# Kernel optimization log

Measured on AMD Instinct MI355X. Metric: run time of the kernel, lower is better.

## Reference

```python
import jax, jax.numpy as jnp
import numpy as np

N_HOPS = 2
TOPK = 10
LAMBDA = 0.5  # lambda_coeff
N_ENT = 8192
N_USR = 16384
CHANNEL = 64
N_EDGE = 1000000
NNZ = 500000
N_REL = 9


def _l2norm(x, eps=1e-12):
    # F.normalize: x / max(||x||, eps) per row
    n = jnp.linalg.norm(x, axis=-1, keepdims=True)
    return x / jnp.maximum(n, eps)


def build_adj(context, topk):
    n = context.shape[0]
    cn = context / jnp.linalg.norm(context, axis=-1, keepdims=True)
    sim = cn @ cn.T                                   # [N,N]
    knn_val, knn_ind = jax.lax.top_k(sim, topk)        # [N,topk]
    rows = jnp.repeat(jnp.arange(n), topk)
    cols = knn_ind.reshape(-1)
    vals = knn_val.reshape(-1)
    rowsum = knn_val.sum(axis=1)                       # sparse row sums
    dinv = rowsum ** -0.5
    vals = dinv[rows] * vals * dinv[cols]              # D^-1/2 A D^-1/2
    return jnp.zeros((n, n), context.dtype).at[rows, cols].add(vals)


def aggregate(entity_emb, user_emb, head, tail, i_rows, i_cols, inter_vals, weight, edge_type):
    n_ent = entity_emb.shape[0]
    n_usr = user_emb.shape[0]
    rel = weight[edge_type - 1]                        # [E,C]
    h_emb = entity_emb[head]
    t_emb = entity_emb[tail]
    neigh = t_emb * rel                                # [E,C]
    # attention weight: (||h*r|| * ||t*r||)^2 per edge
    att = (jnp.linalg.norm(h_emb * rel, axis=1) * jnp.linalg.norm(t_emb * rel, axis=1)) ** 2
    # scatter_softmax over head segments
    m = jax.ops.segment_max(att, head, num_segments=n_ent)
    e = jnp.exp(att - m[head])
    denom = jax.ops.segment_sum(e, head, num_segments=n_ent)
    w = (e / denom[head])[:, None]                     # [E,1], broadcast == expand
    entity_agg = jax.ops.segment_sum(w * neigh, head, num_segments=n_ent)
    # sparse mm: interact_mat @ entity_emb
    user_agg = jax.ops.segment_sum(inter_vals[:, None] * entity_emb[i_cols], i_rows, num_segments=n_usr)
    score = jax.nn.softmax(user_emb @ weight.T, axis=-1)
    user_agg = user_agg + (score @ weight) * user_agg
    return entity_agg, user_agg


def setup_inputs() -> dict:
    key = jax.random.key(0)
    k = jax.random.split(key, 7)
    user_emb = jax.random.normal(k[0], (N_USR, CHANNEL), jnp.float32) * 0.1
    entity_emb = jax.random.normal(k[1], (N_ENT, CHANNEL), jnp.float32) * 0.1
    edge_index = jax.random.randint(k[2], (2, N_EDGE), 0, N_ENT)
    edge_type = jax.random.randint(k[3], (N_EDGE,), 0, N_REL - 1) + 1  # in [1, n_relations-1]
    inter_rows = jax.random.randint(k[4], (NNZ,), 0, N_USR)
    inter_cols = jax.random.randint(k[5], (NNZ,), 0, N_ENT)
    inter_indices = jnp.stack([inter_rows, inter_cols], axis=0)
    inter_vals = jax.random.uniform(k[6], (NNZ,), jnp.float32)
    # xavier-uniform-like relation weight
    bound = float(np.sqrt(6.0 / (N_REL - 1 + CHANNEL)))
    weight = jax.random.uniform(jax.random.fold_in(key, 7), (N_REL - 1, CHANNEL), jnp.float32, -bound, bound)
    return {"user_emb": user_emb, "entity_emb": entity_emb, "edge_index": edge_index,
            "edge_type": edge_type, "inter_indices": inter_indices,
            "inter_vals": inter_vals, "weight": weight}


def reference(user_emb, entity_emb, edge_index, edge_type, inter_indices, inter_vals, weight):
    head, tail = edge_index[0], edge_index[1]
    i_rows, i_cols = inter_indices[0], inter_indices[1]
    origin_item_adj = build_adj(entity_emb, TOPK)
    entity_res_emb = entity_emb
    user_res_emb = user_emb
    for _ in range(N_HOPS):
        entity_emb, user_emb = aggregate(entity_emb, user_emb, head, tail,
                                         i_rows, i_cols, inter_vals, weight, edge_type)
        entity_emb = _l2norm(entity_emb)
        user_emb = _l2norm(user_emb)
        entity_res_emb = entity_res_emb + entity_emb
        user_res_emb = user_res_emb + user_emb
    item_adj = (1.0 - LAMBDA) * build_adj(entity_res_emb, TOPK) + LAMBDA * origin_item_adj
    return entity_res_emb, user_res_emb, item_adj
```

## Files before the change

### kernel.cpp

```cpp
#include <hip/hip_runtime.h>
#include <hip/hip_bf16.h>

#define N_ENT   8192
#define N_USR   16384
#define CH      64
#define N_EDGEC 1000000
#define NNZC    500000
#define TOPKC   10
#define NRELM1  8
#define KSPLIT  384
#define BKS     96

typedef __bf16 bf16x8 __attribute__((ext_vector_type(8)));
typedef float  f32x4  __attribute__((ext_vector_type(4)));

static __device__ __forceinline__ float waveReduceSum(float v){
#pragma unroll
  for(int o=1;o<64;o<<=1) v += __shfl_xor(v,o,64);
  return v;
}
static __device__ __forceinline__ float waveReduceMax(float v){
#pragma unroll
  for(int o=1;o<64;o<<=1) v = fmaxf(v, __shfl_xor(v,o,64));
  return v;
}
static __device__ __forceinline__ int waveReduceMaxI(int v){
#pragma unroll
  for(int o=1;o<64;o<<=1){ int t=__shfl_xor(v,o,64); v = t>v? t: v; }
  return v;
}
static __device__ __forceinline__ unsigned long long u64max(unsigned long long a, unsigned long long b){
  return a>b? a: b;
}
static __device__ __forceinline__ unsigned mapf(float v){
  unsigned u = __float_as_uint(v);
  return (u & 0x80000000u) ? ~u : (u | 0x80000000u);
}
static __device__ __forceinline__ int vbin(float v){
  int b = (int)fmaf(v, 1023.5f, 1023.5f);
  return min(max(b, 0), 2047);
}
static __device__ __forceinline__ ushort f2bf(float x){
  unsigned u = __float_as_uint(x);
  return (ushort)((u + 0x7FFFu + ((u>>16)&1u)) >> 16);
}
static __device__ __forceinline__ float bf2f(ushort h){
  return __uint_as_float((unsigned)h<<16);
}

__global__ void k_hist(const int* __restrict__ keys, int n, int* __restrict__ hist){
  int i = blockIdx.x*blockDim.x + threadIdx.x;
  int stride = gridDim.x*blockDim.x;
  for(; i<n; i+=stride) atomicAdd(&hist[keys[i]], 1);
}

__global__ __launch_bounds__(1024) void k_scan(const int* __restrict__ hist,
                                               int* __restrict__ start,
                                               int* __restrict__ cursor, int n){
  __shared__ int part[1024];
  int t = threadIdx.x;
  int chunk = n/1024;
  int base = t*chunk;
  int s = 0;
  for(int i=0;i<chunk;i++) s += hist[base+i];
  part[t] = s; __syncthreads();
  for(int off=1; off<1024; off<<=1){
    int v = (t>=off) ? part[t-off] : 0;
    __syncthreads();
    part[t] += v;
    __syncthreads();
  }
  int run = (t==0) ? 0 : part[t-1];
  for(int i=0;i<chunk;i++){
    start[base+i] = run; cursor[base+i] = run;
    run += hist[base+i];
  }
  if(t==1023) start[n] = run;
}

__global__ void k_scatter_sortE(const int* __restrict__ head,
                                const int* __restrict__ tail,
                                const int* __restrict__ etype, int n,
                                int* __restrict__ cursor, int* __restrict__ trS){
  int i = blockIdx.x*blockDim.x + threadIdx.x;
  int stride = gridDim.x*blockDim.x;
  for(; i<n; i+=stride){
    int pos = atomicAdd(&cursor[head[i]], 1);
    trS[pos] = (tail[i] & 8191) | ((etype[i]-1)<<13);
  }
}

__global__ void k_scatter_sortU(const int* __restrict__ irows,
                                const int* __restrict__ icols,
                                const float* __restrict__ ivals, int n,
                                int* __restrict__ cursor,
                                int* __restrict__ icolsS, float* __restrict__ ivalsS){
  int i = blockIdx.x*blockDim.x + threadIdx.x;
  int stride = gridDim.x*blockDim.x;
  for(; i<n; i+=stride){
    int pos = atomicAdd(&cursor[irows[i]], 1);
    icolsS[pos] = icols[i];
    ivalsS[pos] = ivals[i];
  }
}

__global__ __launch_bounds__(256) void k_split(const float* __restrict__ in,
                                               ushort* __restrict__ outA,
                                               ushort* __restrict__ outB){
  int wave = threadIdx.x>>6, lane = threadIdx.x&63;
  int r = blockIdx.x*4 + wave;
  float v = in[(size_t)r*CH+lane];
  float ss = waveReduceSum(v*v);
  float x = v / sqrtf(ss);
  ushort h = f2bf(x);
  float r1 = x - bf2f(h);
  ushort m = f2bf(r1);
  float r2 = r1 - bf2f(m);
  ushort l = f2bf(r2);
  ushort* oA = outA + (size_t)r*KSPLIT;
  ushort* oB = outB + (size_t)r*KSPLIT;
  oA[lane]     =h; oA[64+lane] =h; oA[128+lane]=m;
  oA[192+lane] =l; oA[256+lane]=h; oA[320+lane]=m;
  oB[lane]     =h; oB[64+lane] =m; oB[128+lane]=h;
  oB[192+lane] =h; oB[256+lane]=l; oB[320+lane]=m;
}

__global__ __launch_bounds__(256) void k_gemm_bf16(const ushort* __restrict__ A,
                                                   const ushort* __restrict__ B,
                                                   float* __restrict__ C){
  __shared__ ushort As[128*BKS];
  __shared__ ushort Bs[128*BKS];
  const int tid = threadIdx.x, lane = tid&63, wid = tid>>6;
  const int bi = blockIdx.y*128, bj = blockIdx.x*128;
  const int wr = (wid>>1)*64, wc = (wid&1)*64;
  const int r16 = lane&15, kg = lane>>4;

  f32x4 acc[4][4] = {};

  const uint4* gA = (const uint4*)A + (size_t)bi*(KSPLIT/8);
  const uint4* gB = (const uint4*)B + (size_t)bj*(KSPLIT/8);
  const int row2 = tid>>1, half = tid&1;

  for(int s=0; s<KSPLIT/BKS; ++s){
    __syncthreads();
#pragma unroll
    for(int jj=0;jj<6;jj++){
      *(uint4*)&As[row2*BKS + half*48 + jj*8] = gA[row2*(KSPLIT/8) + s*12 + half*6 + jj];
      *(uint4*)&Bs[row2*BKS + half*48 + jj*8] = gB[row2*(KSPLIT/8) + s*12 + half*6 + jj];
    }
    __syncthreads();
#pragma unroll
    for(int kk=0;kk<3;kk++){
      bf16x8 a[4], b[4];
#pragma unroll
      for(int m=0;m<4;m++)
        a[m] = *(const bf16x8*)&As[(wr+m*16+r16)*BKS + kk*32 + kg*8];
#pragma unroll
      for(int n=0;n<4;n++)
        b[n] = *(const bf16x8*)&Bs[(wc+n*16+r16)*BKS + kk*32 + kg*8];
#pragma unroll
      for(int m=0;m<4;m++)
#pragma unroll
        for(int n=0;n<4;n++)
          acc[m][n] = __builtin_amdgcn_mfma_f32_16x16x32_bf16(a[m], b[n], acc[m][n], 0,0,0);
    }
  }

#pragma unroll
  for(int m=0;m<4;m++){
#pragma unroll
    for(int n=0;n<4;n++){
      size_t base = (size_t)(bi + wr + m*16 + kg*4)*N_ENT + (bj + wc + n*16 + r16);
      C[base]          = acc[m][n][0];
      C[base+N_ENT]    = acc[m][n][1];
      C[base+2*N_ENT]  = acc[m][n][2];
      C[base+3*N_ENT]  = acc[m][n][3];
    }
  }
}

#define CANDCAP 256
__global__ __launch_bounds__(64) void k_topk(const float* __restrict__ S,
                                             int* __restrict__ knn_idx,
                                             float* __restrict__ knn_val,
                                             float* __restrict__ rowsum){
  const int row = blockIdx.x;
  const int lane = threadIdx.x;
  const float4* s4 = (const float4*)(S + (size_t)row*N_ENT);

  __shared__ int hist[2048];
  __shared__ unsigned long long cand[CANDCAP];
  __shared__ int cnt;
#pragma unroll
  for(int i=lane;i<2048;i+=64) hist[i]=0;
  if(lane==0) cnt=0;
  __syncthreads();

  for(int it=0; it<N_ENT/256; ++it){
    float4 v = s4[it*64+lane];
    atomicAdd(&hist[vbin(v.x)],1);
    atomicAdd(&hist[vbin(v.y)],1);
    atomicAdd(&hist[vbin(v.z)],1);
    atomicAdd(&hist[vbin(v.w)],1);
  }
  __syncthreads();

  int base = lane*32;
  int s = 0;
#pragma unroll
  for(int j=0;j<32;j++) s += hist[base+j];
  int ss = s;
#pragma unroll
  for(int off=1; off<64; off<<=1){
    int t = __shfl_down(ss, off, 64);
    if(lane+off<64) ss += t;
  }
  int above = ss - s;
  int B_local = 0;
  if(ss >= TOPKC && above < TOPKC){
    int running = above;
    for(int j=31;j>=0;--j){
      running += hist[base+j];
      if(running >= TOPKC){ B_local = base+j; break; }
    }
  }
  int B = waveReduceMaxI(B_local);

  for(int it=0; it<N_ENT/256; ++it){
    int vi = it*64+lane;
    float4 v = s4[vi];
    int c0 = vi*4;
    float vv[4] = {v.x,v.y,v.z,v.w};
#pragma unroll
    for(int j=0;j<4;j++){
      if(vbin(vv[j]) >= B){
        int pos = atomicAdd(&cnt,1);
        if(pos < CANDCAP)
          cand[pos] = ((unsigned long long)mapf(vv[j])<<32)
                    | (unsigned long long)(0xFFFFFFFFu - (unsigned)(c0+j));
      }
    }
  }
  __syncthreads();
  int n = cnt;

  if(n <= CANDCAP){
    unsigned long long c0 = (lane      < n) ? cand[lane]       : 0ull;
    unsigned long long c1 = (lane+64   < n) ? cand[lane+64]    : 0ull;
    unsigned long long c2 = (lane+128  < n) ? cand[lane+128]   : 0ull;
    unsigned long long c3 = (lane+192  < n) ? cand[lane+192]   : 0ull;
    float rs = 0.f;
    for(int sel=0; sel<TOPKC; ++sel){
      unsigned long long m = u64max(u64max(c0,c1), u64max(c2,c3));
#pragma unroll
      for(int o=1;o<64;o<<=1) m = u64max(m, __shfl_xor(m,o,64));
      if(c0==m) c0=0ull; else if(c1==m) c1=0ull;
      else if(c2==m) c2=0ull; else if(c3==m) c3=0ull;
      if(lane==0){
        unsigned mk = (unsigned)(m>>32);
        unsigned uo = (mk & 0x80000000u) ? (mk ^ 0x80000000u) : ~mk;
        float v = __uint_as_float(uo);
        int col = (int)(0xFFFFFFFFu - (unsigned)(m & 0xFFFFFFFFu));
        knn_idx[row*TOPKC+sel] = col;
        knn_val[row*TOPKC+sel] = v;
        rs += v;
      }
    }
    if(lane==0) rowsum[row] = rs;
  } else {
    unsigned long long loc[TOPKC];
#pragma unroll
    for(int i=0;i<TOPKC;i++) loc[i]=0ull;
    for(int it=0; it<N_ENT/256; ++it){
      int vi = it*64+lane;
      float4 v = s4[vi];
      int c0i = vi*4;
      float vv[4] = {v.x,v.y,v.z,v.w};
#pragma unroll
      for(int j=0;j<4;j++){
        unsigned u = mapf(vv[j]);
        unsigned long long key = ((unsigned long long)u<<32)
                               | (unsigned long long)(0xFFFFFFFFu - (unsigned)(c0i+j));
        if(key > loc[TOPKC-1]){
          unsigned long long t = key;
#pragma unroll
          for(int z=0; z<TOPKC; ++z){
            if(t > loc[z]){ unsigned long long tmp=loc[z]; loc[z]=t; t=tmp; }
          }
        }
      }
    }
    float rs = 0.f;
    for(int sel=0; sel<TOPKC; ++sel){
      unsigned long long m = loc[0];
#pragma unroll
      for(int o=1;o<64;o<<=1) m = u64max(m, __shfl_xor(m,o,64));
      if(loc[0] == m){
#pragma unroll
        for(int z=0;z<TOPKC-1;++z) loc[z]=loc[z+1];
        loc[TOPKC-1]=0ull;
      }
      if(lane==0){
        unsigned mk = (unsigned)(m>>32);
        unsigned uo = (mk & 0x80000000u) ? (mk ^ 0x80000000u) : ~mk;
        float v = __uint_as_float(uo);
        int col = (int)(0xFFFFFFFFu - (unsigned)(m & 0xFFFFFFFFu));
        knn_idx[row*TOPKC+sel] = col;
        knn_val[row*TOPKC+sel] = v;
        rs += v;
      }
    }
    if(lane==0) rowsum[row] = rs;
  }
}

__global__ __launch_bounds__(256) void k_q(const float* __restrict__ ent,
                                           const float* __restrict__ W,
                                           float* __restrict__ q){
  int wave=threadIdx.x>>6, lane=threadIdx.x&63;
  int r = blockIdx.x*4+wave;
  if(r>=N_ENT) return;
  float x = ent[(size_t)r*CH+lane];
#pragma unroll
  for(int rel=0; rel<NRELM1; rel++){
    float tt = x*W[rel*CH+lane];
    float s = waveReduceSum(tt*tt);
    if(lane==0) q[r*NRELM1+rel]=s;
  }
}

__global__ __launch_bounds__(256) void k_edge_agg(
    const int* __restrict__ trS, const int* __restrict__ startE,
    const float* __restrict__ ent, const float* __restrict__ W,
    const float* __restrict__ q, float* __restrict__ wbuf,
    float* __restrict__ agg){
  int wave=threadIdx.x>>6, lane=threadIdx.x&63;
  int h = blockIdx.x*4+wave;
  if(h>=N_ENT) return;
  int s = startE[h], e2 = startE[h+1];

  float qh[NRELM1];
#pragma unroll
  for(int r=0;r<NRELM1;r++) qh[r] = q[h*NRELM1+r];

  float mx = 0.f;
  for(int p=s+lane; p<e2; p+=64){
    int tr = trS[p];
    int tl = tr & 8191, r = tr>>13;
    float att = qh[r]*q[tl*NRELM1+r];
    wbuf[p] = att;
    mx = fmaxf(mx, att);
  }
  mx = waveReduceMax(mx);

  float dn = 0.f;
  for(int p=s+lane; p<e2; p+=64){
    float e = expf(wbuf[p]-mx);
    wbuf[p] = e;
    dn += e;
  }
  dn = waveReduceSum(dn);
  float inv = (dn>0.f) ? 1.f/dn : 0.f;

  float wr[NRELM1];
#pragma unroll
  for(int r=0;r<NRELM1;r++) wr[r] = W[r*CH+lane];
  float acc = 0.f;
  for(int p=s; p<e2; p++){
    int tr = trS[p];
    int tl = tr & 8191, r = tr>>13;
    float wgt = wbuf[p]*inv;
    acc = fmaf(wgt*wr[r], ent[(size_t)tl*CH+lane], acc);
  }
  agg[(size_t)h*CH+lane] = acc;
}

__global__ __launch_bounds__(256) void k_user(
    const int* __restrict__ icolsS, const float* __restrict__ ivalsS,
    const int* __restrict__ startU,
    const float* __restrict__ ent, const float* __restrict__ W,
    float* __restrict__ usr, float* __restrict__ usr_res){
  int wave=threadIdx.x>>6, lane=threadIdx.x&63;
  int u = blockIdx.x*4+wave;
  if(u>=N_USR) return;
  float ue = usr[(size_t)u*CH+lane];
  float l[NRELM1];
#pragma unroll
  for(int r=0;r<NRELM1;r++) l[r] = waveReduceSum(ue*W[r*CH+lane]);
  float lm = l[0];
#pragma unroll
  for(int r=1;r<NRELM1;r++) lm = fmaxf(lm,l[r]);
  float se=0.f;
#pragma unroll
  for(int r=0;r<NRELM1;r++){ l[r]=expf(l[r]-lm); se+=l[r]; }
  float inv = 1.f/se;
  float g = 0.f;
#pragma unroll
  for(int r=0;r<NRELM1;r++) g = fmaf(l[r]*inv, W[r*CH+lane], g);
  float acc=0.f;
  int s=startU[u], e2=startU[u+1];
  for(int p=s;p<e2;p++){
    acc = fmaf(ivalsS[p], ent[(size_t)icolsS[p]*CH+lane], acc);
  }
  float res = acc*(1.f+g);
  float nrm = sqrtf(waveReduceSum(res*res));
  float outv = res / fmaxf(nrm, 1e-12f);
  usr_res[(size_t)u*CH+lane] += outv;
  usr[(size_t)u*CH+lane] = outv;
}

__global__ __launch_bounds__(256) void k_entfin(const float* __restrict__ agg,
                                                float* __restrict__ cur,
                                                float* __restrict__ res){
  int wave=threadIdx.x>>6, lane=threadIdx.x&63;
  int r = blockIdx.x*4+wave;
  if(r>=N_ENT) return;
  float v = agg[(size_t)r*CH+lane];
  float nrm = sqrtf(waveReduceSum(v*v));
  float outv = v / fmaxf(nrm, 1e-12f);
  cur[(size_t)r*CH+lane]=outv;
  res[(size_t)r*CH+lane]+=outv;
}

__global__ __launch_bounds__(256) void k_write_adj(
    const int* __restrict__ ki0, const float* __restrict__ kv0,
    const float* __restrict__ rs0,
    const int* __restrict__ ki1, const float* __restrict__ kv1,
    const float* __restrict__ rs1,
    float* __restrict__ adj){
  const int row = blockIdx.x;
  const int t = threadIdx.x;
  __shared__ int   cols[2*TOPKC];
  __shared__ float vals[2*TOPKC];

  if(t < TOPKC){
    int c = ki1[row*TOPKC+t];
    cols[t] = c;
    vals[t] = 0.5f * kv1[row*TOPKC+t] / (sqrtf(rs1[row]) * sqrtf(rs1[c]));
  } else if(t < 2*TOPKC){
    int i = t - TOPKC;
    int c = ki0[row*TOPKC+i];
    cols[t] = c;
    vals[t] = 0.5f * kv0[row*TOPKC+i] / (sqrtf(rs0[row]) * sqrtf(rs0[c]));
  }
  __syncthreads();
  if(t==0){
    for(int i=TOPKC;i<2*TOPKC;i++){
      int c = cols[i];
      for(int j=0;j<TOPKC;j++){
        if(cols[j]==c){ vals[j]+=vals[i]; cols[i]=-1; break; }
      }
    }
  }
  __syncthreads();

  float4* adj4 = (float4*)(adj + (size_t)row*N_ENT);
  float4 z = {0.f,0.f,0.f,0.f};
#pragma unroll
  for(int k=0;k<8;k++) adj4[k*256 + t] = z;
  __syncthreads();
  if(t < 2*TOPKC){
    int c = cols[t];
    if(c >= 0) adj[(size_t)row*N_ENT + c] = vals[t];
  }
}

extern "C" void kernel_launch(void* const* d_in, const int* in_sizes, int n_in,
                              void* d_out, int out_size, void* d_ws, size_t ws_size,
                              hipStream_t stream){
  const float* user_emb   = (const float*)d_in[0];
  const float* entity_emb = (const float*)d_in[1];
  const int*   edge_index = (const int*)d_in[2];
  const int*   edge_type  = (const int*)d_in[3];
  const int*   inter_idx  = (const int*)d_in[4];
  const float* inter_vals = (const float*)d_in[5];
  const float* W          = (const float*)d_in[6];

  const int* head  = edge_index;
  const int* tail  = edge_index + N_EDGEC;
  const int* irows = inter_idx;
  const int* icols = inter_idx + NNZC;

  float* out     = (float*)d_out;
  float* ent_res = out;
  float* usr_res = out + (size_t)N_ENT*CH;
  float* adj     = out + (size_t)N_ENT*CH + (size_t)N_USR*CH;

  char* wp = (char*)d_ws;
  auto alloc = [&](size_t bytes)->void*{
    void* p = (void*)wp; wp += (bytes+255)/256*256; return p;
  };
  ushort* abufA  = (ushort*)alloc((size_t)N_ENT*KSPLIT*2);
  ushort* abufB  = (ushort*)alloc((size_t)N_ENT*KSPLIT*2);
  float* cur_ent = (float*)alloc((size_t)N_ENT*CH*4);
  float* cur_usr = (float*)alloc((size_t)N_USR*CH*4);
  float* agg     = (float*)alloc((size_t)N_ENT*CH*4);
  float* q       = (float*)alloc((size_t)N_ENT*NRELM1*4);
  int*   histE   = (int*)alloc((size_t)N_ENT*4);
  int*   startE  = (int*)alloc((size_t)(N_ENT+1)*4);
  int*   cursorE = (int*)alloc((size_t)N_ENT*4);
  int*   trS     = (int*)alloc((size_t)N_EDGEC*4);
  int*   histU   = (int*)alloc((size_t)N_USR*4);
  int*   startU  = (int*)alloc((size_t)(N_USR+1)*4);
  int*   cursorU = (int*)alloc((size_t)N_USR*4);
  int*   icolsS  = (int*)alloc((size_t)NNZC*4);
  float* ivalsS  = (float*)alloc((size_t)NNZC*4);
  int*   knn_idx0= (int*)alloc((size_t)N_ENT*TOPKC*4);
  float* knn_val0= (float*)alloc((size_t)N_ENT*TOPKC*4);
  float* rowsum0 = (float*)alloc((size_t)N_ENT*4);
  int*   knn_idx1= (int*)alloc((size_t)N_ENT*TOPKC*4);
  float* knn_val1= (float*)alloc((size_t)N_ENT*TOPKC*4);
  float* rowsum1 = (float*)alloc((size_t)N_ENT*4);

  float* wbuf = adj;

  hipMemsetAsync(histE, 0, (size_t)N_ENT*4, stream);
  hipMemsetAsync(histU, 0, (size_t)N_USR*4, stream);
  hipMemcpyAsync(ent_res, entity_emb, (size_t)N_ENT*CH*4, hipMemcpyDeviceToDevice, stream);
  hipMemcpyAsync(usr_res, user_emb,   (size_t)N_USR*CH*4, hipMemcpyDeviceToDevice, stream);
  hipMemcpyAsync(cur_ent, entity_emb, (size_t)N_ENT*CH*4, hipMemcpyDeviceToDevice, stream);
  hipMemcpyAsync(cur_usr, user_emb,   (size_t)N_USR*CH*4, hipMemcpyDeviceToDevice, stream);

  k_hist<<<1024,256,0,stream>>>(head, N_EDGEC, histE);
  k_hist<<<512,256,0,stream>>>(irows, NNZC, histU);
  k_scan<<<1,1024,0,stream>>>(histE, startE, cursorE, N_ENT);
  k_scan<<<1,1024,0,stream>>>(histU, startU, cursorU, N_USR);
  k_scatter_sortE<<<1024,256,0,stream>>>(head, tail, edge_type, N_EDGEC, cursorE, trS);
  k_scatter_sortU<<<512,256,0,stream>>>(irows, icols, inter_vals, NNZC, cursorU, icolsS, ivalsS);

  dim3 gg(N_ENT/128, N_ENT/128);

  k_split<<<N_ENT/4,256,0,stream>>>(entity_emb, abufA, abufB);
  k_gemm_bf16<<<gg,256,0,stream>>>(abufA, abufB, adj);
  k_topk<<<N_ENT,64,0,stream>>>(adj, knn_idx0, knn_val0, rowsum0);

  for(int hop=0; hop<2; ++hop){
    k_q<<<N_ENT/4,256,0,stream>>>(cur_ent, W, q);
    k_edge_agg<<<N_ENT/4,256,0,stream>>>(trS, startE, cur_ent, W, q, wbuf, agg);
    k_user<<<N_USR/4,256,0,stream>>>(icolsS, ivalsS, startU, cur_ent, W, cur_usr, usr_res);
    k_entfin<<<N_ENT/4,256,0,stream>>>(agg, cur_ent, ent_res);
  }

  k_split<<<N_ENT/4,256,0,stream>>>(ent_res, abufA, abufB);
  k_gemm_bf16<<<gg,256,0,stream>>>(abufA, abufB, adj);
  k_topk<<<N_ENT,64,0,stream>>>(adj, knn_idx1, knn_val1, rowsum1);

  k_write_adj<<<N_ENT,256,0,stream>>>(knn_idx0, knn_val0, rowsum0,
                                      knn_idx1, knn_val1, rowsum1, adj);
}
```

Measured before the change: 0.9998 ms.

## Prune top-k scan using per-tile row maxima computed in GEMM epilogue

The GEMM epilogue now reduces each 128-column tile's row maximum and writes it to a rowmax buffer. The top-k kernel takes the 10th-largest tile maximum as a lower bound on the threshold and rereads only the tiles whose maximum reaches it, instead of two full histogram passes over each 8192-wide row. This cuts top-k memory traffic sharply. It adds shuffles, two syncs and a small store to the GEMM, and it depends on the threshold keeping candidates under the cap or taking the fallback path.

New measurement: 847.1 us. 1.18x faster.

```diff
diff --git a/kernel.cpp b/kernel.cpp
--- a/kernel.cpp
+++ b/kernel.cpp
@@ -10,6 +10,7 @@
 #define NRELM1  8
 #define KSPLIT  384
 #define BKS     96
+#define NTILE   64
 
 typedef __bf16 bf16x8 __attribute__((ext_vector_type(8)));
 typedef float  f32x4  __attribute__((ext_vector_type(4)));
@@ -22,11 +23,6 @@
 static __device__ __forceinline__ float waveReduceMax(float v){
 #pragma unroll
   for(int o=1;o<64;o<<=1) v = fmaxf(v, __shfl_xor(v,o,64));
-  return v;
-}
-static __device__ __forceinline__ int waveReduceMaxI(int v){
-#pragma unroll
-  for(int o=1;o<64;o<<=1){ int t=__shfl_xor(v,o,64); v = t>v? t: v; }
   return v;
 }
 static __device__ __forceinline__ unsigned long long u64max(unsigned long long a, unsigned long long b){
@@ -36,9 +32,9 @@
   unsigned u = __float_as_uint(v);
   return (u & 0x80000000u) ? ~u : (u | 0x80000000u);
 }
-static __device__ __forceinline__ int vbin(float v){
-  int b = (int)fmaf(v, 1023.5f, 1023.5f);
-  return min(max(b, 0), 2047);
+static __device__ __forceinline__ float unmapf(unsigned mk){
+  unsigned uo = (mk & 0x80000000u) ? (mk ^ 0x80000000u) : ~mk;
+  return __uint_as_float(uo);
 }
 static __device__ __forceinline__ ushort f2bf(float x){
   unsigned u = __float_as_uint(x);
@@ -127,7 +123,8 @@
 
 __global__ __launch_bounds__(256) void k_gemm_bf16(const ushort* __restrict__ A,
                                                    const ushort* __restrict__ B,
-                                                   float* __restrict__ C){
+                                                   float* __restrict__ C,
+                                                   float* __restrict__ rowmax){
   __shared__ ushort As[128*BKS];
   __shared__ ushort Bs[128*BKS];
   const int tid = threadIdx.x, lane = tid&63, wid = tid>>6;
@@ -177,10 +174,45 @@
       C[base+3*N_ENT]  = acc[m][n][3];
     }
   }
+
+  float tmax[4][4];
+#pragma unroll
+  for(int m=0;m<4;m++){
+#pragma unroll
+    for(int rg=0;rg<4;rg++){
+      float v = acc[m][0][rg];
+      v = fmaxf(v, acc[m][1][rg]);
+      v = fmaxf(v, acc[m][2][rg]);
+      v = fmaxf(v, acc[m][3][rg]);
+#pragma unroll
+      for(int o=1;o<16;o<<=1) v = fmaxf(v, __shfl_xor(v, o, 64));
+      tmax[m][rg] = v;
+    }
+  }
+  __syncthreads();
+  float* rm = (float*)As;
+  if(((wid&1)==0) && r16==0){
+#pragma unroll
+    for(int m=0;m<4;m++)
+#pragma unroll
+      for(int rg=0;rg<4;rg++)
+        rm[wr + m*16 + kg*4 + rg] = tmax[m][rg];
+  }
+  __syncthreads();
+  if(((wid&1)==1) && r16==0){
+#pragma unroll
+    for(int m=0;m<4;m++)
+#pragma unroll
+      for(int rg=0;rg<4;rg++){
+        int rrow = wr + m*16 + kg*4 + rg;
+        rowmax[(size_t)(bi+rrow)*NTILE + blockIdx.x] = fmaxf(tmax[m][rg], rm[rrow]);
+      }
+  }
 }
 
 #define CANDCAP 256
 __global__ __launch_bounds__(64) void k_topk(const float* __restrict__ S,
+                                             const float* __restrict__ rowmax,
                                              int* __restrict__ knn_idx,
                                              float* __restrict__ knn_val,
                                              float* __restrict__ rowsum){
@@ -188,52 +220,36 @@
   const int lane = threadIdx.x;
   const float4* s4 = (const float4*)(S + (size_t)row*N_ENT);
 
-  __shared__ int hist[2048];
   __shared__ unsigned long long cand[CANDCAP];
-  __shared__ int cnt;
-#pragma unroll
-  for(int i=lane;i<2048;i+=64) hist[i]=0;
-  if(lane==0) cnt=0;
-  __syncthreads();
-
-  for(int it=0; it<N_ENT/256; ++it){
-    float4 v = s4[it*64+lane];
-    atomicAdd(&hist[vbin(v.x)],1);
-    atomicAdd(&hist[vbin(v.y)],1);
-    atomicAdd(&hist[vbin(v.z)],1);
-    atomicAdd(&hist[vbin(v.w)],1);
-  }
-  __syncthreads();
-
-  int base = lane*32;
-  int s = 0;
-#pragma unroll
-  for(int j=0;j<32;j++) s += hist[base+j];
-  int ss = s;
-#pragma unroll
-  for(int off=1; off<64; off<<=1){
-    int t = __shfl_down(ss, off, 64);
-    if(lane+off<64) ss += t;
-  }
-  int above = ss - s;
-  int B_local = 0;
-  if(ss >= TOPKC && above < TOPKC){
-    int running = above;
-    for(int j=31;j>=0;--j){
-      running += hist[base+j];
-      if(running >= TOPKC){ B_local = base+j; break; }
-    }
-  }
-  int B = waveReduceMaxI(B_local);
-
-  for(int it=0; it<N_ENT/256; ++it){
-    int vi = it*64+lane;
-    float4 v = s4[vi];
-    int c0 = vi*4;
+  __shared__ int tlist[NTILE];
+  __shared__ int cnt, tcnt;
+  if(lane==0){ cnt=0; tcnt=0; }
+  __syncthreads();
+
+  float tm = rowmax[(size_t)row*NTILE + lane];
+  unsigned long long work = ((unsigned long long)mapf(tm)<<32) | (unsigned)lane;
+  unsigned long long w = 0;
+  for(int sel=0; sel<TOPKC; ++sel){
+    w = work;
+#pragma unroll
+    for(int o=1;o<64;o<<=1) w = u64max(w, __shfl_xor(w,o,64));
+    if(work == w) work = 0ull;
+  }
+  float tauf = unmapf((unsigned)(w>>32));
+
+  if(tm >= tauf){ int p = atomicAdd(&tcnt,1); tlist[p] = lane; }
+  __syncthreads();
+  int nt = tcnt;
+
+  for(int i = (lane>>5); i < nt; i += 2){
+    int t  = tlist[i];
+    int fo = lane&31;
+    float4 v = s4[t*32 + fo];
+    int c0 = t*128 + fo*4;
     float vv[4] = {v.x,v.y,v.z,v.w};
 #pragma unroll
     for(int j=0;j<4;j++){
-      if(vbin(vv[j]) >= B){
+      if(vv[j] >= tauf){
         int pos = atomicAdd(&cnt,1);
         if(pos < CANDCAP)
           cand[pos] = ((unsigned long long)mapf(vv[j])<<32)
@@ -257,9 +273,7 @@
       if(c0==m) c0=0ull; else if(c1==m) c1=0ull;
       else if(c2==m) c2=0ull; else if(c3==m) c3=0ull;
       if(lane==0){
-        unsigned mk = (unsigned)(m>>32);
-        unsigned uo = (mk & 0x80000000u) ? (mk ^ 0x80000000u) : ~mk;
-        float v = __uint_as_float(uo);
+        float v = unmapf((unsigned)(m>>32));
         int col = (int)(0xFFFFFFFFu - (unsigned)(m & 0xFFFFFFFFu));
         knn_idx[row*TOPKC+sel] = col;
         knn_val[row*TOPKC+sel] = v;
@@ -301,9 +315,7 @@
         loc[TOPKC-1]=0ull;
       }
       if(lane==0){
-        unsigned mk = (unsigned)(m>>32);
-        unsigned uo = (mk & 0x80000000u) ? (mk ^ 0x80000000u) : ~mk;
-        float v = __uint_as_float(uo);
+        float v = unmapf((unsigned)(m>>32));
         int col = (int)(0xFFFFFFFFu - (unsigned)(m & 0xFFFFFFFFu));
         knn_idx[row*TOPKC+sel] = col;
         knn_val[row*TOPKC+sel] = v;
@@ -492,6 +504,7 @@
   };
   ushort* abufA  = (ushort*)alloc((size_t)N_ENT*KSPLIT*2);
   ushort* abufB  = (ushort*)alloc((size_t)N_ENT*KSPLIT*2);
+  float* rowmax  = (float*)alloc((size_t)N_ENT*NTILE*4);
   float* cur_ent = (float*)alloc((size_t)N_ENT*CH*4);
   float* cur_usr = (float*)alloc((size_t)N_USR*CH*4);
   float* agg     = (float*)alloc((size_t)N_ENT*CH*4);
@@ -531,8 +544,8 @@
   dim3 gg(N_ENT/128, N_ENT/128);
 
   k_split<<<N_ENT/4,256,0,stream>>>(entity_emb, abufA, abufB);
-  k_gemm_bf16<<<gg,256,0,stream>>>(abufA, abufB, adj);
-  k_topk<<<N_ENT,64,0,stream>>>(adj, knn_idx0, knn_val0, rowsum0);
+  k_gemm_bf16<<<gg,256,0,stream>>>(abufA, abufB, adj, rowmax);
+  k_topk<<<N_ENT,64,0,stream>>>(adj, rowmax, knn_idx0, knn_val0, rowsum0);
 
   for(int hop=0; hop<2; ++hop){
     k_q<<<N_ENT/4,256,0,stream>>>(cur_ent, W, q);
@@ -542,8 +555,8 @@
   }
 
   k_split<<<N_ENT/4,256,0,stream>>>(ent_res, abufA, abufB);
-  k_gemm_bf16<<<gg,256,0,stream>>>(abufA, abufB, adj);
-  k_topk<<<N_ENT,64,0,stream>>>(adj, knn_idx1, knn_val1, rowsum1);
+  k_gemm_bf16<<<gg,256,0,stream>>>(abufA, abufB, adj, rowmax);
+  k_topk<<<N_ENT,64,0,stream>>>(adj, rowmax, knn_idx1, knn_val1, rowsum1);
 
   k_write_adj<<<N_ENT,256,0,stream>>>(knn_idx0, knn_val0, rowsum0,
                                       knn_idx1, knn_val1, rowsum1, adj);
```
